# Performance work log

Hardware: AMD Instinct MI355X
Metric: run time of the kernel (lower is better)

Reference implementation:

```python
import jax, jax.numpy as jnp
import numpy as np

N = 10000
E = 160000
D_IN = 128
H = 1024
NUM_GRAPHS = 8
EPS = 1e-5


def setup_inputs() -> dict:
    key = jax.random.key(0)
    ks = jax.random.split(key, 24)
    x = jax.random.normal(ks[0], (N, D_IN), dtype=jnp.float32)
    edge_index = jax.random.randint(ks[1], (2, E), 0, N, dtype=jnp.int32)
    batch = jnp.sort(jax.random.randint(ks[2], (N,), 0, NUM_GRAPHS, dtype=jnp.int32))
    s = 0.02
    W1 = jax.random.normal(ks[3], (D_IN, H), dtype=jnp.float32) * s
    b1 = jnp.zeros((H,), jnp.float32)
    Wh = jax.random.normal(ks[4], (3, H, H), dtype=jnp.float32) * s
    bh = jnp.zeros((3, H), jnp.float32)
    ln_g = jnp.ones((4, H), jnp.float32)
    ln_b = jnp.zeros((4, H), jnp.float32)
    vW = jax.random.normal(ks[5], (6, H, H), dtype=jnp.float32) * s
    vb = jnp.zeros((6, H), jnp.float32)
    vWo = jax.random.normal(ks[6], (H, 1), dtype=jnp.float32) * s
    vbo = jnp.zeros((1,), jnp.float32)
    return {"x": x, "edge_index": edge_index, "batch": batch,
            "W1": W1, "b1": b1, "Wh": Wh, "bh": bh,
            "ln_g": ln_g, "ln_b": ln_b, "vW": vW, "vb": vb,
            "vWo": vWo, "vbo": vbo}


def _layer_norm(x, g, b):
    m = jnp.mean(x, axis=-1, keepdims=True)
    v = jnp.mean(jnp.square(x - m), axis=-1, keepdims=True)
    return (x - m) * jax.lax.rsqrt(v + EPS) * g + b


def reference(x, edge_index, batch, W1, b1, Wh, bh, ln_g, ln_b, vW, vb, vWo, vbo):
    # GCNConv: add self loops, symmetric normalization, x @ W, scatter-add at dst, + bias
    loops = jnp.arange(N, dtype=edge_index.dtype)
    src = jnp.concatenate([edge_index[0], loops])
    dst = jnp.concatenate([edge_index[1], loops])
    deg = jax.ops.segment_sum(jnp.ones_like(dst, dtype=x.dtype), dst, num_segments=N)
    dinv = jax.lax.rsqrt(jnp.maximum(deg, 1.0))
    norm = (dinv[src] * dinv[dst])[:, None]  # [E+N, 1]

    def gcn(h, W, b):
        h = h @ W                              # [N, H]
        msg = h[src] * norm                    # gather + scale [E+N, H]
        return jax.ops.segment_sum(msg, dst, num_segments=N) + b

    x1 = gcn(x, W1, b1)
    h = jax.nn.relu(_layer_norm(x1, ln_g[0], ln_b[0]))
    x2 = gcn(h, Wh[0], bh[0])
    h = jax.nn.relu(_layer_norm(x2 + x1, ln_g[1], ln_b[1]))
    x3 = gcn(h, Wh[1], bh[1])
    h = jax.nn.relu(_layer_norm(x3 + x1, ln_g[2], ln_b[2]))
    x4 = gcn(h, Wh[2], bh[2])
    node_embeddings = jax.nn.relu(_layer_norm(x4 + h, ln_g[3], ln_b[3]))

    # global mean pool per graph
    counts = jax.ops.segment_sum(jnp.ones((N,), x.dtype), batch, num_segments=NUM_GRAPHS)
    sums = jax.ops.segment_sum(node_embeddings, batch, num_segments=NUM_GRAPHS)
    graph_embedding = sums / jnp.maximum(counts, 1.0)[:, None]

    v = graph_embedding
    for i in range(6):
        v = jax.nn.relu(v @ vW[i] + vb[i])
    state_value = (v @ vWo + vbo).squeeze(-1)
    return node_embeddings, graph_embedding, state_value
```

## Files before the change

kernel.cpp:

```cpp
#include <hip/hip_runtime.h>
#include <stdint.h>

#define N_NODES 10000
#define E_EDGES 160000
#define DIN 128
#define H 1024
#define NUM_GRAPHS 8
#define LN_EPS 1e-5f

typedef unsigned short u16;
typedef __attribute__((ext_vector_type(8))) short short8;
typedef __attribute__((ext_vector_type(8))) unsigned short ushort8v;
typedef __attribute__((ext_vector_type(4))) float f32x4;

__device__ __forceinline__ float bf2f(u16 v) { return __uint_as_float(((unsigned)v) << 16); }
__device__ __forceinline__ u16 f2bf(float f) {
    unsigned u = __float_as_uint(f);
    u += 0x7fffu + ((u >> 16) & 1u);
    return (u16)(u >> 16);
}

__global__ void k_init(int* cnt, int* goff, float* __restrict__ gsum,
                       float* __restrict__ vbuf, const float* __restrict__ vb) {
    int i = blockIdx.x * 256 + threadIdx.x;
    if (i < N_NODES) cnt[i] = 0;
    if (i <= NUM_GRAPHS) goff[i] = 0;
    if (i < NUM_GRAPHS * H) gsum[i] = 0.f;
    if (i < 6 * H) {
        int il = i >> 10, j = i & (H - 1);
        float b = vb[il * H + j];
        float* base = vbuf + (size_t)(il + 1) * NUM_GRAPHS * H;
#pragma unroll
        for (int g = 0; g < NUM_GRAPHS; g++) base[g * H + j] = b;
    }
}

__global__ void k_count(const int* __restrict__ dst, int* __restrict__ cnt) {
    int e = blockIdx.x * 256 + threadIdx.x;
    if (e < E_EDGES) atomicAdd(&cnt[dst[e]], 1);
}

__global__ __launch_bounds__(1024) void k_scan(const int* __restrict__ cnt, int* __restrict__ offs,
                                               int* __restrict__ cursor, float* __restrict__ dinv) {
    __shared__ int s[1024];
    __shared__ int carry_s;
    int tid = threadIdx.x;
    if (tid == 0) carry_s = 0;
    __syncthreads();
    for (int base = 0; base < N_NODES; base += 1024) {
        int i = base + tid;
        int v = (i < N_NODES) ? cnt[i] : 0;
        s[tid] = v;
        __syncthreads();
        for (int off = 1; off < 1024; off <<= 1) {
            int t = (tid >= off) ? s[tid - off] : 0;
            __syncthreads();
            s[tid] += t;
            __syncthreads();
        }
        int incl = s[tid];
        int excl = incl - v;
        int cbase = carry_s;
        if (i < N_NODES) {
            offs[i] = cbase + excl;
            cursor[i] = cbase + excl;
            dinv[i] = rsqrtf((float)(v + 1));
        }
        __syncthreads();
        if (tid == 1023) carry_s = cbase + incl;
        __syncthreads();
    }
    if (tid == 0) offs[N_NODES] = carry_s;
}

__global__ void k_fill(const int* __restrict__ src, const int* __restrict__ dst,
                       int* __restrict__ cursor, int* __restrict__ csr_src) {
    int e = blockIdx.x * 256 + threadIdx.x;
    if (e < E_EDGES) {
        int d = dst[e];
        int slot = atomicAdd(&cursor[d], 1);
        csr_src[slot] = src[e];
    }
}

__global__ void k_gbound(const int* __restrict__ batch, int* __restrict__ goff) {
    int i = blockIdx.x * 256 + threadIdx.x;
    if (i >= N_NODES) return;
    int b0 = batch[i];
    int b1 = (i + 1 < N_NODES) ? batch[i + 1] : NUM_GRAPHS;
    for (int g = b0 + 1; g <= b1; g++) goff[g] = i + 1;
}

__global__ void k_cvt(const float* __restrict__ src, u16* __restrict__ dst, int n) {
    int i = blockIdx.x * 256 + threadIdx.x;
    if (i < n) dst[i] = f2bf(src[i]);
}

__global__ void k_transpose_cvt(const float* __restrict__ src, u16* __restrict__ dst, int R, int C) {
    __shared__ float tile[32][33];
    int tx = threadIdx.x, ty = threadIdx.y;
    int x = blockIdx.x * 32 + tx;
#pragma unroll
    for (int i = 0; i < 32; i += 8) {
        int y = blockIdx.y * 32 + ty + i;
        tile[ty + i][tx] = (y < R && x < C) ? src[(size_t)y * C + x] : 0.f;
    }
    __syncthreads();
    int xo = blockIdx.y * 32 + tx;
#pragma unroll
    for (int i = 0; i < 32; i += 8) {
        int yo = blockIdx.x * 32 + ty + i;
        if (yo < C && xo < R) dst[(size_t)yo * R + xo] = f2bf(tile[tx][ty + i]);
    }
}

typedef __attribute__((address_space(1))) const unsigned int gas_u32;
typedef __attribute__((address_space(3))) unsigned int las_u32;
__device__ __forceinline__ void gld_lds16(const void* g, void* l) {
    __builtin_amdgcn_global_load_lds((gas_u32*)g, (las_u32*)l, 16, 0, 0);
}

__global__ __launch_bounds__(256) void k_gemm(const u16* __restrict__ A, const u16* __restrict__ B,
                                              u16* __restrict__ C, int M, int Nn, int K) {
    __shared__ __align__(16) u16 sA[128 * 32];
    __shared__ __align__(16) u16 sB[128 * 32];
    int tid = threadIdx.x;
    int lane = tid & 63;
    int w = tid >> 6;
    int wm = w >> 1, wn = w & 1;
    int m0 = blockIdx.x * 128;
    int n0 = blockIdx.y * 128;

    f32x4 zero = {0.f, 0.f, 0.f, 0.f};
    f32x4 acc[4][4];
#pragma unroll
    for (int i = 0; i < 4; i++)
#pragma unroll
        for (int j = 0; j < 4; j++) acc[i][j] = zero;

    int srow = w * 32 + (lane >> 2);
    int scol = (lane & 3) * 8;
    u16* laA = sA + w * 1024;
    u16* laB = sB + w * 1024;

    for (int k0 = 0; k0 < K; k0 += 32) {
        __syncthreads();
#pragma unroll
        for (int q = 0; q < 2; q++) {
            int rA = m0 + srow + q * 16;
            rA = rA < M ? rA : M - 1;
            gld_lds16(A + (size_t)rA * K + k0 + scol, laA + q * 512);
            gld_lds16(B + (size_t)(n0 + srow + q * 16) * K + k0 + scol, laB + q * 512);
        }
        __syncthreads();

        short8 af[4], bv[4];
#pragma unroll
        for (int mi = 0; mi < 4; mi++)
            af[mi] = *(const short8*)(sA + (wm * 64 + mi * 16 + (lane & 15)) * 32 + (lane >> 4) * 8);
#pragma unroll
        for (int ni = 0; ni < 4; ni++)
            bv[ni] = *(const short8*)(sB + (wn * 64 + ni * 16 + (lane & 15)) * 32 + (lane >> 4) * 8);
#pragma unroll
        for (int mi = 0; mi < 4; mi++)
#pragma unroll
            for (int ni = 0; ni < 4; ni++)
                acc[mi][ni] = __builtin_amdgcn_mfma_f32_16x16x32_bf16(af[mi], bv[ni], acc[mi][ni], 0, 0, 0);
    }

    int rbase = m0 + wm * 64 + (lane >> 4) * 4;
    int cbase = n0 + wn * 64 + (lane & 15);
#pragma unroll
    for (int mi = 0; mi < 4; mi++) {
#pragma unroll
        for (int r = 0; r < 4; r++) {
            int row = rbase + mi * 16 + r;
            if (row < M) {
#pragma unroll
                for (int ni = 0; ni < 4; ni++)
                    C[(size_t)row * Nn + cbase + ni * 16] = f2bf(acc[mi][ni][r]);
            }
        }
    }
}

template <int MODE>
__global__ __launch_bounds__(128) void k_agg_ln(const u16* __restrict__ t, const u16* __restrict__ resid,
                                                const float* __restrict__ bias, const float* __restrict__ gamma,
                                                const float* __restrict__ beta, const float* __restrict__ dinv,
                                                const int* __restrict__ offs, const int* __restrict__ csr_src,
                                                u16* __restrict__ out_bf, u16* __restrict__ out_pre,
                                                float* __restrict__ out_f32) {
    __shared__ float s_dv[128];
    __shared__ int s_id[128];
    __shared__ float red1[2], red2[2];
    int d = blockIdx.x;
    int tid = threadIdx.x;
    int c = tid * 8;
    float dd = dinv[d];

    float a[8];
    {
        ushort8v v = *(const ushort8v*)(t + (size_t)d * H + c);
#pragma unroll
        for (int i = 0; i < 8; i++) a[i] = dd * bf2f(v[i]);
    }
    int beg = offs[d], end = offs[d + 1];
    for (int chunk = beg; chunk < end; chunk += 128) {
        int nthis = end - chunk;
        if (nthis > 128) nthis = 128;
        __syncthreads();
        if (tid < nthis) {
            int s = csr_src[chunk + tid];
            s_id[tid] = s;
            s_dv[tid] = dinv[s];
        }
        __syncthreads();
        for (int i = 0; i < nthis; i++) {
            int s = s_id[i];
            float ds = s_dv[i];
            ushort8v v = *(const ushort8v*)(t + (size_t)s * H + c);
#pragma unroll
            for (int j = 0; j < 8; j++) a[j] += ds * bf2f(v[j]);
        }
    }
    float x[8];
#pragma unroll
    for (int i = 0; i < 8; i++) x[i] = dd * a[i] + bias[c + i];
    if (MODE >= 1) {
        ushort8v r = *(const ushort8v*)(resid + (size_t)d * H + c);
#pragma unroll
        for (int i = 0; i < 8; i++) x[i] += bf2f(r[i]);
    }
    if (MODE == 0) {
        ushort8v p;
#pragma unroll
        for (int i = 0; i < 8; i++) p[i] = f2bf(x[i]);
        *(ushort8v*)(out_pre + (size_t)d * H + c) = p;
    }
    float s1 = 0.f, s2 = 0.f;
#pragma unroll
    for (int i = 0; i < 8; i++) { s1 += x[i]; s2 += x[i] * x[i]; }
#pragma unroll
    for (int off = 32; off > 0; off >>= 1) {
        s1 += __shfl_down(s1, off);
        s2 += __shfl_down(s2, off);
    }
    int lane = tid & 63, wv = tid >> 6;
    if (lane == 0) { red1[wv] = s1; red2[wv] = s2; }
    __syncthreads();
    float sum = red1[0] + red1[1];
    float ssq = red2[0] + red2[1];
    float mean = sum * (1.f / H);
    float var = fmaxf(ssq * (1.f / H) - mean * mean, 0.f);
    float inv = rsqrtf(var + LN_EPS);
    float y[8];
#pragma unroll
    for (int i = 0; i < 8; i++)
        y[i] = fmaxf((x[i] - mean) * inv * gamma[c + i] + beta[c + i], 0.f);
    if (MODE == 2) {
        float4 o0 = {y[0], y[1], y[2], y[3]};
        float4 o1 = {y[4], y[5], y[6], y[7]};
        *(float4*)(out_f32 + (size_t)d * H + c) = o0;
        *(float4*)(out_f32 + (size_t)d * H + c + 4) = o1;
    } else {
        ushort8v o;
#pragma unroll
        for (int i = 0; i < 8; i++) o[i] = f2bf(y[i]);
        *(ushort8v*)(out_bf + (size_t)d * H + c) = o;
    }
}

#define PC_NODES 16
__global__ __launch_bounds__(256) void k_pool_acc(const float* __restrict__ ne, const int* __restrict__ batch,
                                                  float* __restrict__ gsum) {
    int c = blockIdx.x * 256 + threadIdx.x;
    int nbeg = blockIdx.y * PC_NODES;
    int nend = nbeg + PC_NODES;
    if (nend > N_NODES) nend = N_NODES;
    float acc = 0.f;
    int curg = batch[nbeg];
    for (int n = nbeg; n < nend; n++) {
        int g = batch[n];
        if (g != curg) {
            atomicAdd(&gsum[curg * H + c], acc);
            acc = 0.f;
            curg = g;
        }
        acc += ne[(size_t)n * H + c];
    }
    atomicAdd(&gsum[curg * H + c], acc);
}

__global__ __launch_bounds__(256) void k_pool_fin(const float* __restrict__ gsum, const int* __restrict__ goff,
                                                  float* __restrict__ v0, float* __restrict__ ge_out) {
    int g = blockIdx.y;
    int c = blockIdx.x * 256 + threadIdx.x;
    float cntf = (float)(goff[g + 1] - goff[g]);
    float m = gsum[g * H + c] / fmaxf(cntf, 1.f);
    v0[g * H + c] = m;
    ge_out[(size_t)g * H + c] = m;
}

template <bool RELU_IN>
__global__ __launch_bounds__(256) void k_mlp_acc(const float* __restrict__ vin, const float* __restrict__ W,
                                                 float* __restrict__ vout) {
    __shared__ float sk[64];
    int g = blockIdx.y;
    int j = blockIdx.x * 256 + threadIdx.x;
    int k0 = blockIdx.z * 64;
    if (threadIdx.x < 64) {
        float v = vin[g * H + k0 + threadIdx.x];
        sk[threadIdx.x] = RELU_IN ? fmaxf(v, 0.f) : v;
    }
    __syncthreads();
    float acc = 0.f;
#pragma unroll
    for (int k = 0; k < 64; k++) acc += sk[k] * W[(size_t)(k0 + k) * H + j];
    atomicAdd(&vout[g * H + j], acc);
}

__global__ void k_head(const float* __restrict__ vin, const float* __restrict__ Wo,
                       const float* __restrict__ bo, float* __restrict__ out) {
    int g = blockIdx.x;
    int tid = threadIdx.x;
    float s = 0.f;
    for (int k = tid; k < H; k += 256) s += fmaxf(vin[g * H + k], 0.f) * Wo[k];
#pragma unroll
    for (int off = 32; off > 0; off >>= 1) s += __shfl_down(s, off);
    __shared__ float p[4];
    if ((tid & 63) == 0) p[tid >> 6] = s;
    __syncthreads();
    if (tid == 0) out[g] = p[0] + p[1] + p[2] + p[3] + bo[0];
}

extern "C" void kernel_launch(void* const* d_in, const int* in_sizes, int n_in,
                              void* d_out, int out_size, void* d_ws, size_t ws_size,
                              hipStream_t stream) {
    const float* x = (const float*)d_in[0];
    const int* ei = (const int*)d_in[1];
    const int* batch = (const int*)d_in[2];
    const float* W1 = (const float*)d_in[3];
    const float* b1 = (const float*)d_in[4];
    const float* Wh = (const float*)d_in[5];
    const float* bh = (const float*)d_in[6];
    const float* ln_g = (const float*)d_in[7];
    const float* ln_b = (const float*)d_in[8];
    const float* vW = (const float*)d_in[9];
    const float* vb = (const float*)d_in[10];
    const float* vWo = (const float*)d_in[11];
    const float* vbo = (const float*)d_in[12];
    const int* esrc = ei;
    const int* edst = ei + E_EDGES;

    char* ws = (char*)d_ws;
    size_t off = 0;
    auto carve = [&](size_t bytes) -> char* {
        char* p = ws + off;
        off += (bytes + 255) & ~(size_t)255;
        return p;
    };
    float* dinv = (float*)carve(N_NODES * 4);
    int* cnt = (int*)carve(N_NODES * 4);
    int* offs = (int*)carve((N_NODES + 1) * 4);
    int* cursor = (int*)carve(N_NODES * 4);
    int* csr_src = (int*)carve(E_EDGES * 4);
    int* goff = (int*)carve((NUM_GRAPHS + 1) * 4);
    float* gsum = (float*)carve(NUM_GRAPHS * H * 4);
    float* vbuf = (float*)carve((size_t)7 * NUM_GRAPHS * H * 4);
    u16* xb = (u16*)carve((size_t)N_NODES * DIN * 2);
    u16* Wt = (u16*)carve((size_t)H * H * 2);
    u16* tbuf = (u16*)carve((size_t)N_NODES * H * 2);
    u16* hbuf = (u16*)carve((size_t)N_NODES * H * 2);
    u16* x1buf = (u16*)carve((size_t)N_NODES * H * 2);

    float* out_ne = (float*)d_out;
    float* out_ge = out_ne + (size_t)N_NODES * H;
    float* out_sv = out_ge + (size_t)NUM_GRAPHS * H;

    k_init<<<(N_NODES + 255) / 256, 256, 0, stream>>>(cnt, goff, gsum, vbuf, vb);
    k_count<<<(E_EDGES + 255) / 256, 256, 0, stream>>>(edst, cnt);
    k_scan<<<1, 1024, 0, stream>>>(cnt, offs, cursor, dinv);
    k_fill<<<(E_EDGES + 255) / 256, 256, 0, stream>>>(esrc, edst, cursor, csr_src);
    k_gbound<<<(N_NODES + 255) / 256, 256, 0, stream>>>(batch, goff);
    k_cvt<<<(N_NODES * DIN + 255) / 256, 256, 0, stream>>>(x, xb, N_NODES * DIN);

    dim3 tb(32, 8);
    dim3 gg((N_NODES + 127) / 128, H / 128);

    k_transpose_cvt<<<dim3(H / 32, DIN / 32), tb, 0, stream>>>(W1, Wt, DIN, H);
    k_gemm<<<gg, 256, 0, stream>>>(xb, Wt, tbuf, N_NODES, H, DIN);
    k_agg_ln<0><<<N_NODES, 128, 0, stream>>>(tbuf, nullptr, b1, ln_g, ln_b, dinv, offs, csr_src,
                                             hbuf, x1buf, nullptr);

    k_transpose_cvt<<<dim3(H / 32, H / 32), tb, 0, stream>>>(Wh + 0 * (size_t)H * H, Wt, H, H);
    k_gemm<<<gg, 256, 0, stream>>>(hbuf, Wt, tbuf, N_NODES, H, H);
    k_agg_ln<1><<<N_NODES, 128, 0, stream>>>(tbuf, x1buf, bh, ln_g + H, ln_b + H, dinv, offs, csr_src,
                                             hbuf, nullptr, nullptr);

    k_transpose_cvt<<<dim3(H / 32, H / 32), tb, 0, stream>>>(Wh + 1 * (size_t)H * H, Wt, H, H);
    k_gemm<<<gg, 256, 0, stream>>>(hbuf, Wt, tbuf, N_NODES, H, H);
    k_agg_ln<1><<<N_NODES, 128, 0, stream>>>(tbuf, x1buf, bh + H, ln_g + 2 * H, ln_b + 2 * H, dinv, offs, csr_src,
                                             hbuf, nullptr, nullptr);

    k_transpose_cvt<<<dim3(H / 32, H / 32), tb, 0, stream>>>(Wh + 2 * (size_t)H * H, Wt, H, H);
    k_gemm<<<gg, 256, 0, stream>>>(hbuf, Wt, tbuf, N_NODES, H, H);
    k_agg_ln<2><<<N_NODES, 128, 0, stream>>>(tbuf, hbuf, bh + 2 * H, ln_g + 3 * H, ln_b + 3 * H, dinv, offs, csr_src,
                                             nullptr, nullptr, out_ne);

    k_pool_acc<<<dim3(H / 256, (N_NODES + PC_NODES - 1) / PC_NODES), 256, 0, stream>>>(out_ne, batch, gsum);
    k_pool_fin<<<dim3(H / 256, NUM_GRAPHS), 256, 0, stream>>>(gsum, goff, vbuf, out_ge);

    dim3 mg(H / 256, NUM_GRAPHS, 16);
    k_mlp_acc<false><<<mg, 256, 0, stream>>>(vbuf, vW, vbuf + (size_t)1 * NUM_GRAPHS * H);
    for (int i = 1; i < 6; i++)
        k_mlp_acc<true><<<mg, 256, 0, stream>>>(vbuf + (size_t)i * NUM_GRAPHS * H, vW + (size_t)i * H * H,
                                                vbuf + (size_t)(i + 1) * NUM_GRAPHS * H);
    k_head<<<NUM_GRAPHS, 256, 0, stream>>>(vbuf + (size_t)6 * NUM_GRAPHS * H, vWo, vbo, out_sv);
}
```

Measured before the change: 538.9 us.

## Aggregate input features before first GCN GEMM; unroll gather loop and warp-shuffle scan

For the first GCN layer, neighbour aggregation is done on the 128-wide input features before the GEMM, using the identity A(XW) = (AX)W. The 1024-wide gather that used to follow the GEMM becomes a plain bias+LayerNorm kernel, which removes most of that layer's gather traffic. The remaining gather loops are unrolled by 4 with padded dummy entries so more loads are in flight, and the prefix scan now uses wave shuffles instead of a shared-memory loop with many barriers. Rounding the aggregated input to bf16 before the GEMM changes numerics slightly.

```diff
diff --git a/kernel.cpp b/kernel.cpp
--- a/kernel.cpp
+++ b/kernel.cpp
@@ -42,32 +42,43 @@
 
 __global__ __launch_bounds__(1024) void k_scan(const int* __restrict__ cnt, int* __restrict__ offs,
                                                int* __restrict__ cursor, float* __restrict__ dinv) {
-    __shared__ int s[1024];
+    __shared__ int wsum[16];
     __shared__ int carry_s;
     int tid = threadIdx.x;
+    int lane = tid & 63, wv = tid >> 6;
     if (tid == 0) carry_s = 0;
     __syncthreads();
     for (int base = 0; base < N_NODES; base += 1024) {
         int i = base + tid;
         int v = (i < N_NODES) ? cnt[i] : 0;
-        s[tid] = v;
-        __syncthreads();
-        for (int off = 1; off < 1024; off <<= 1) {
-            int t = (tid >= off) ? s[tid - off] : 0;
-            __syncthreads();
-            s[tid] += t;
-            __syncthreads();
-        }
-        int incl = s[tid];
+        int x = v;
+#pragma unroll
+        for (int off = 1; off < 64; off <<= 1) {
+            int t = __shfl_up(x, off);
+            if (lane >= off) x += t;
+        }
+        if (lane == 63) wsum[wv] = x;
+        __syncthreads();
+        int carry = carry_s;
+        if (wv == 0) {
+            int ws = (lane < 16) ? wsum[lane] : 0;
+#pragma unroll
+            for (int off = 1; off < 16; off <<= 1) {
+                int t = __shfl_up(ws, off);
+                if (lane >= off) ws += t;
+            }
+            if (lane < 16) wsum[lane] = ws;
+        }
+        __syncthreads();
+        int wbase = (wv > 0) ? wsum[wv - 1] : 0;
+        int incl = wbase + x;
         int excl = incl - v;
-        int cbase = carry_s;
         if (i < N_NODES) {
-            offs[i] = cbase + excl;
-            cursor[i] = cbase + excl;
+            offs[i] = carry + excl;
+            cursor[i] = carry + excl;
             dinv[i] = rsqrtf((float)(v + 1));
         }
-        __syncthreads();
-        if (tid == 1023) carry_s = cbase + incl;
+        if (tid == 1023) carry_s = carry + incl;
         __syncthreads();
     }
     if (tid == 0) offs[N_NODES] = carry_s;
@@ -112,6 +123,100 @@
         int yo = blockIdx.x * 32 + ty + i;
         if (yo < C && xo < R) dst[(size_t)yo * R + xo] = f2bf(tile[tx][ty + i]);
     }
+}
+
+__global__ __launch_bounds__(64) void k_agg_x(const u16* __restrict__ xb, const float* __restrict__ dinv,
+                                              const int* __restrict__ offs, const int* __restrict__ csr_src,
+                                              u16* __restrict__ xa) {
+    __shared__ float s_dv[64];
+    __shared__ int s_id[64];
+    int d = blockIdx.x;
+    int tid = threadIdx.x;
+    int c = tid * 2;
+    float dd = dinv[d];
+    float a0, a1;
+    {
+        unsigned v = *(const unsigned*)(xb + (size_t)d * DIN + c);
+        a0 = dd * bf2f((u16)(v & 0xffffu));
+        a1 = dd * bf2f((u16)(v >> 16));
+    }
+    int beg = offs[d], end = offs[d + 1];
+    for (int chunk = beg; chunk < end; chunk += 64) {
+        int nthis = end - chunk;
+        if (nthis > 64) nthis = 64;
+        int np = (nthis + 7) & ~7;
+        __syncthreads();
+        if (tid < nthis) {
+            int s = csr_src[chunk + tid];
+            s_id[tid] = s;
+            s_dv[tid] = dinv[s];
+        } else if (tid < np) {
+            s_id[tid] = d;
+            s_dv[tid] = 0.f;
+        }
+        __syncthreads();
+        for (int i = 0; i < np; i += 8) {
+            unsigned v[8];
+            float e[8];
+#pragma unroll
+            for (int u = 0; u < 8; u++) {
+                int s = s_id[i + u];
+                e[u] = s_dv[i + u];
+                v[u] = *(const unsigned*)(xb + (size_t)s * DIN + c);
+            }
+#pragma unroll
+            for (int u = 0; u < 8; u++) {
+                a0 += e[u] * bf2f((u16)(v[u] & 0xffffu));
+                a1 += e[u] * bf2f((u16)(v[u] >> 16));
+            }
+        }
+    }
+    a0 *= dd;
+    a1 *= dd;
+    unsigned o = ((unsigned)f2bf(a1) << 16) | (unsigned)f2bf(a0);
+    *(unsigned*)(xa + (size_t)d * DIN + c) = o;
+}
+
+__global__ __launch_bounds__(128) void k_ln1(const u16* __restrict__ t, const float* __restrict__ bias,
+                                             const float* __restrict__ gamma, const float* __restrict__ beta,
+                                             u16* __restrict__ out_bf, u16* __restrict__ out_pre) {
+    __shared__ float red1[2], red2[2];
+    int d = blockIdx.x;
+    int tid = threadIdx.x;
+    int c = tid * 8;
+    float x[8];
+    {
+        ushort8v v = *(const ushort8v*)(t + (size_t)d * H + c);
+#pragma unroll
+        for (int i = 0; i < 8; i++) x[i] = bf2f(v[i]) + bias[c + i];
+    }
+    {
+        ushort8v p;
+#pragma unroll
+        for (int i = 0; i < 8; i++) p[i] = f2bf(x[i]);
+        *(ushort8v*)(out_pre + (size_t)d * H + c) = p;
+    }
+    float s1 = 0.f, s2 = 0.f;
+#pragma unroll
+    for (int i = 0; i < 8; i++) { s1 += x[i]; s2 += x[i] * x[i]; }
+#pragma unroll
+    for (int off = 32; off > 0; off >>= 1) {
+        s1 += __shfl_down(s1, off);
+        s2 += __shfl_down(s2, off);
+    }
+    int lane = tid & 63, wv = tid >> 6;
+    if (lane == 0) { red1[wv] = s1; red2[wv] = s2; }
+    __syncthreads();
+    float sum = red1[0] + red1[1];
+    float ssq = red2[0] + red2[1];
+    float mean = sum * (1.f / H);
+    float var = fmaxf(ssq * (1.f / H) - mean * mean, 0.f);
+    float inv = rsqrtf(var + LN_EPS);
+    ushort8v o;
+#pragma unroll
+    for (int i = 0; i < 8; i++)
+        o[i] = f2bf(fmaxf((x[i] - mean) * inv * gamma[c + i] + beta[c + i], 0.f));
+    *(ushort8v*)(out_bf + (size_t)d * H + c) = o;
 }
 
 typedef __attribute__((address_space(1))) const unsigned int gas_u32;
@@ -209,19 +314,27 @@
     for (int chunk = beg; chunk < end; chunk += 128) {
         int nthis = end - chunk;
         if (nthis > 128) nthis = 128;
+        int np = (nthis + 3) & ~3;
         __syncthreads();
         if (tid < nthis) {
             int s = csr_src[chunk + tid];
             s_id[tid] = s;
             s_dv[tid] = dinv[s];
-        }
-        __syncthreads();
-        for (int i = 0; i < nthis; i++) {
-            int s = s_id[i];
-            float ds = s_dv[i];
-            ushort8v v = *(const ushort8v*)(t + (size_t)s * H + c);
-#pragma unroll
-            for (int j = 0; j < 8; j++) a[j] += ds * bf2f(v[j]);
+        } else if (tid < np) {
+            s_id[tid] = d;
+            s_dv[tid] = 0.f;
+        }
+        __syncthreads();
+        for (int i = 0; i < np; i += 4) {
+            int s0 = s_id[i + 0], s1 = s_id[i + 1], s2 = s_id[i + 2], s3 = s_id[i + 3];
+            float e0 = s_dv[i + 0], e1 = s_dv[i + 1], e2 = s_dv[i + 2], e3 = s_dv[i + 3];
+            ushort8v v0 = *(const ushort8v*)(t + (size_t)s0 * H + c);
+            ushort8v v1 = *(const ushort8v*)(t + (size_t)s1 * H + c);
+            ushort8v v2 = *(const ushort8v*)(t + (size_t)s2 * H + c);
+            ushort8v v3 = *(const ushort8v*)(t + (size_t)s3 * H + c);
+#pragma unroll
+            for (int j = 0; j < 8; j++)
+                a[j] += e0 * bf2f(v0[j]) + e1 * bf2f(v1[j]) + e2 * bf2f(v2[j]) + e3 * bf2f(v3[j]);
         }
     }
     float x[8];
@@ -369,6 +482,7 @@
     float* gsum = (float*)carve(NUM_GRAPHS * H * 4);
     float* vbuf = (float*)carve((size_t)7 * NUM_GRAPHS * H * 4);
     u16* xb = (u16*)carve((size_t)N_NODES * DIN * 2);
+    u16* xa = (u16*)carve((size_t)N_NODES * DIN * 2);
     u16* Wt = (u16*)carve((size_t)H * H * 2);
     u16* tbuf = (u16*)carve((size_t)N_NODES * H * 2);
     u16* hbuf = (u16*)carve((size_t)N_NODES * H * 2);
@@ -388,10 +502,10 @@
     dim3 tb(32, 8);
     dim3 gg((N_NODES + 127) / 128, H / 128);
 
+    k_agg_x<<<N_NODES, 64, 0, stream>>>(xb, dinv, offs, csr_src, xa);
     k_transpose_cvt<<<dim3(H / 32, DIN / 32), tb, 0, stream>>>(W1, Wt, DIN, H);
-    k_gemm<<<gg, 256, 0, stream>>>(xb, Wt, tbuf, N_NODES, H, DIN);
-    k_agg_ln<0><<<N_NODES, 128, 0, stream>>>(tbuf, nullptr, b1, ln_g, ln_b, dinv, offs, csr_src,
-                                             hbuf, x1buf, nullptr);
+    k_gemm<<<gg, 256, 0, stream>>>(xa, Wt, tbuf, N_NODES, H, DIN);
+    k_ln1<<<N_NODES, 128, 0, stream>>>(tbuf, b1, ln_g, ln_b, hbuf, x1buf);
 
     k_transpose_cvt<<<dim3(H / 32, H / 32), tb, 0, stream>>>(Wh + 0 * (size_t)H * H, Wt, H, H);
     k_gemm<<<gg, 256, 0, stream>>>(hbuf, Wt, tbuf, N_NODES, H, H);
```

Result: faster. 505.5 us (-6.2%).
